# Performance work log

Hardware: AMD Instinct MI355X
Metric: run time of the kernel (lower is better)

## Reference

```python
import jax, jax.numpy as jnp
import numpy as np

K = 7        # kernal_size
STRIDE = 1
PAD = 3      # padding (reflect)
M = K // 2   # center tap index
GAMA = 0.5
EPS = 1e-09


def interp_linear(x, n_out):
    # torch F.interpolate(mode='linear', align_corners=False) on last dim. x: (b, c, n_in)
    n_in = x.shape[-1]
    src = (jnp.arange(n_out, dtype=jnp.float32) + 0.5) * (n_in / n_out) - 0.5
    src = jnp.clip(src, 0.0, n_in - 1.0)
    lo = jnp.floor(src).astype(jnp.int32)
    hi = jnp.minimum(lo + 1, n_in - 1)
    w = (src - lo.astype(jnp.float32)).astype(x.dtype)
    return x[..., lo] * (1.0 - w) + x[..., hi] * w


def unfold1d(x, k, s, p):
    # x: (b, c, n) -> windows (b, L, c, k), matching F.unfold's c-major/k-minor layout
    if p > 0:
        x = jnp.pad(x, ((0, 0), (0, 0), (p, p)), mode='reflect')
    n = x.shape[-1]
    L = (n - k) // s + 1
    idx = jnp.arange(L)[:, None] * s + jnp.arange(k)[None, :]  # (L, k)
    win = x[:, :, idx]                                          # (b, c, L, k)
    return jnp.transpose(win, (0, 2, 1, 3))                     # (b, L, c, k)


def setup_inputs() -> dict:
    key = jax.random.key(0)
    k1, k2, k3, k4, k5 = jax.random.split(key, 5)
    b, dc, nd = 16, 16, 1024
    c_in, c_out, n = 64, 128, 4096
    deep = jax.random.normal(k1, (b, dc, nd), dtype=jnp.float32)
    x = jax.random.normal(k2, (b, c_in, n), dtype=jnp.float32)
    conv_w = jax.random.normal(k3, (c_in, dc), dtype=jnp.float32) * (1.0 / np.sqrt(dc))
    conv_b = jax.random.normal(k4, (c_in,), dtype=jnp.float32) * 0.02
    fc_w = jax.random.normal(k5, (c_out, c_in * K), dtype=jnp.float32) * (1.0 / np.sqrt(c_in * K))
    return {"deep": deep, "x": x, "conv_w": conv_w, "conv_b": conv_b, "fc_w": fc_w}


def reference(deep, x, conv_w, conv_b, fc_w):
    b, c, n = x.shape
    # --- get_deep_loss ---
    xr = interp_linear(deep, n)                                  # (b, dc, n)
    y = jnp.einsum('bdn,cd->bcn', xr, conv_w) + conv_b[None, :, None]
    mean = jnp.mean(y, axis=2, keepdims=True)
    var = jnp.var(y, axis=2, keepdims=True, ddof=1)              # torch var_mean unbiased
    xs = GAMA * (y - mean) / (var + EPS)                         # DeepShuffle1d
    x1 = unfold1d(xs, K, STRIDE, PAD)                            # (b, L, c, k)
    d = jnp.abs(x1 - x1[..., M:M + 1])
    loss = 1.0 - jnp.tanh(d) ** 2                                # (b, L, c, k)
    alpha = 1.0 / jnp.sum(loss, axis=-1, keepdims=True)          # (b, L, c, 1)
    deep_loss = (loss * alpha).reshape(b, -1, c * K)             # (b, L, c*k)
    # --- deep_conv ---
    y1 = unfold1d(x, K, STRIDE, PAD).reshape(b, -1, c * K)       # (b, L, c*k)
    out = jnp.einsum('blf,of->bol', deep_loss * y1, fc_w)        # (b, c_out, L)
    return out
```

## Files before the change

kernel.cpp:

```cpp
#include <hip/hip_runtime.h>
#include <hip/hip_bf16.h>
#include <math.h>

namespace {
typedef __attribute__((ext_vector_type(8)))  short  short8;
typedef __attribute__((ext_vector_type(4)))  float  floatx4;

constexpr int Bc = 16;
constexpr int DC = 16;
constexpr int ND = 1024;
constexpr int C  = 64;
constexpr int N  = 4096;
constexpr int CO = 128;
constexpr int KW = 7;
constexpr int F  = C * KW;
constexpr int F2 = C * 8;
constexpr int LT = 32;
constexpr int PLD = F2 + 8;
constexpr int GPS = 560;
constexpr int NS = F2 / 32;

constexpr size_t WB_OFF = 0;
constexpr size_t GP_OFF = 262144;
constexpr size_t MC_OFF = 548864;
constexpr size_t SC_OFF = 552960;

constexpr float EXP2_SCALE = 2.8853900817779268f;

__device__ inline unsigned short f2bf(float f) {
    __hip_bfloat16 h = __float2bfloat16(f);
    return __builtin_bit_cast(unsigned short, h);
}
__device__ inline float rcpf(float x) { return __builtin_amdgcn_rcpf(x); }

__global__ __launch_bounds__(256)
void k0(const float* __restrict__ deep, const float* __restrict__ fcw,
        unsigned short* __restrict__ wbs, float* __restrict__ gp)
{
    __shared__ __align__(16) float Dch[DC][132];
    const int blk = blockIdx.x;
    const int tid = threadIdx.x;

    if (blk < 32) {
        const int g    = blk * 256 + tid;
        const int lane = g & 63;
        const int q    = lane >> 4;
        const int rr   = lane & 15;
        const int rest = g >> 6;
        const int t    = rest & 1;
        const int sw   = rest >> 1;
        const int s    = sw & 15;
        const int w    = sw >> 4;
        const int o    = w * 32 + t * 16 + rr;
        const int c    = s * 4 + q;
        const float* src = fcw + o * F + c * KW;
        const float4 v0 = *(const float4*)(src);
        const float4 v1 = *(const float4*)(src + 3);
        short8 h;
        h[0] = (short)f2bf(v0.x); h[1] = (short)f2bf(v0.y);
        h[2] = (short)f2bf(v0.z); h[3] = (short)f2bf(v0.w);
        h[4] = (short)f2bf(v1.y); h[5] = (short)f2bf(v1.z);
        h[6] = (short)f2bf(v1.w); h[7] = 0;
        ((short8*)wbs)[g] = h;
        return;
    }
    const int i2 = blk - 32;
    const int b  = i2 >> 3;
    const int ch = i2 & 7;
    const int t0 = ch * 128;
    const int d  = tid >> 4;
    const int e  = tid & 15;
#pragma unroll
    for (int p = 0; p < 9; ++p) {
        const int tt = e + 16 * p;
        if (tt < 129)
            Dch[d][tt] = deep[(b * DC + d) * ND + min(t0 + tt, ND - 1)];
    }
    __syncthreads();
    float a0 = 0.f, a1 = 0.f, as = 0.f;
    const int n1 = (ch == 7) ? 127 : 128;
    for (int t = 0; t < 128; ++t) {
        const float vd  = Dch[d][t];
        const float ve  = Dch[e][t];
        const float ve1 = (t < n1) ? Dch[e][t + 1] : 0.f;
        a0 = fmaf(vd, ve, a0);
        a1 = fmaf(vd, ve1, a1);
        as += vd;
    }
    float* gpb = gp + (b * 8 + ch) * GPS;
    gpb[tid] = a0;
    gpb[256 + tid] = a1;
    if (e == 0) {
        gpb[512 + d] = as;
        if (ch == 0) gpb[528 + d] = Dch[d][0];
        if (ch == 7) gpb[544 + d] = Dch[d][127];
    }
}

__global__ __launch_bounds__(256)
void ks(const float* __restrict__ gp, const float* __restrict__ conv_w,
        const float* __restrict__ conv_b, float* __restrict__ mcs,
        float* __restrict__ scs)
{
    __shared__ float G0s[256], G1s[256], ss[16], dd0[16], ddN[16], qp[8][64];
    const int b = blockIdx.x, tid = threadIdx.x;
    {
        float a0 = 0.f, a1 = 0.f;
#pragma unroll
        for (int ch = 0; ch < 8; ++ch) {
            const float* gpb = gp + (b * 8 + ch) * GPS;
            a0 += gpb[tid];
            a1 += gpb[256 + tid];
        }
        G0s[tid] = a0; G1s[tid] = a1;
        if (tid < 16) {
            float s = 0.f;
#pragma unroll
            for (int ch = 0; ch < 8; ++ch) s += gp[(b * 8 + ch) * GPS + 512 + tid];
            ss[tid]  = s;
            dd0[tid] = gp[(b * 8 + 0) * GPS + 528 + tid];
            ddN[tid] = gp[(b * 8 + 7) * GPS + 544 + tid];
        }
    }
    __syncthreads();
    const int c = tid & 63, part = tid >> 6;
    float w[DC];
    {
        const float4* wr = (const float4*)(conv_w + c * DC);
#pragma unroll
        for (int p = 0; p < 4; ++p) {
            const float4 v = wr[p];
            w[4 * p] = v.x; w[4 * p + 1] = v.y; w[4 * p + 2] = v.z; w[4 * p + 3] = v.w;
        }
    }
    float q0 = 0.f, q1 = 0.f;
#pragma unroll
    for (int dd = 0; dd < 4; ++dd) {
        const int d = 4 * part + dd;
        float i0 = 0.f, i1 = 0.f;
#pragma unroll
        for (int e = 0; e < DC; ++e) {
            i0 = fmaf(w[e], G0s[d * 16 + e], i0);
            i1 = fmaf(w[e], G1s[d * 16 + e], i1);
        }
        q0 = fmaf(w[d], i0, q0);
        q1 = fmaf(w[d], i1, q1);
    }
    qp[part][c] = q0;
    qp[4 + part][c] = q1;
    __syncthreads();
    if (tid < 64) {
        const float Q0 = qp[0][c] + qp[1][c] + qp[2][c] + qp[3][c];
        const float Q1 = qp[4][c] + qp[5][c] + qp[6][c] + qp[7][c];
        float wS = 0.f, V0 = 0.f, VN = 0.f;
#pragma unroll
        for (int d = 0; d < DC; ++d) {
            wS = fmaf(w[d], ss[d],  wS);
            V0 = fmaf(w[d], dd0[d], V0);
            VN = fmaf(w[d], ddN[d], VN);
        }
        const float cb   = conv_b[c];
        const float mean = wS * (1.f / 1024.f) + cb;
        const float S2   = 2.625f * Q0 + 1.375f * Q1 + 0.6875f * (V0 * V0 + VN * VN)
                         + 8.f * cb * wS + 4096.f * cb * cb;
        const float var  = (S2 - 4096.f * mean * mean) * (1.f / 4095.f);
        mcs[b * 64 + c] = wS * (1.f / 1024.f);
        scs[b * 64 + c] = (0.5f / (var + 1e-9f)) * EXP2_SCALE;
    }
}

__global__ __launch_bounds__(256, 3)
void k2(const float* __restrict__ deep, const float* __restrict__ conv_w,
        const float* __restrict__ x, const float* __restrict__ mcs,
        const float* __restrict__ scs, const unsigned short* __restrict__ wbs,
        float* __restrict__ out)
{
    __shared__ __align__(16) unsigned short phi[LT * PLD];
    __shared__ __align__(16) float Dw[12 * 16];
    const int b   = blockIdx.y;
    const int l0  = blockIdx.x * LT;
    const int t0  = l0 >> 2;
    const int tid = threadIdx.x;
    const int c   = tid & 63;
    const int seg = tid >> 6;

    if (tid < 192) {
        const int ti = tid >> 4, d = tid & 15;
        const int t = min(max(t0 - 2 + ti, 0), ND - 1);
        Dw[ti * 16 + d] = deep[(b * DC + d) * ND + t];
    }
    float w[DC];
    {
        const float4* wr = (const float4*)(conv_w + c * DC);
#pragma unroll
        for (int p = 0; p < 4; ++p) {
            const float4 v = wr[p];
            w[4 * p] = v.x; w[4 * p + 1] = v.y; w[4 * p + 2] = v.z; w[4 * p + 3] = v.w;
        }
    }
    const float mc  = mcs[b * 64 + c];
    const float sc2 = scs[b * 64 + c];

    const int base = l0 + seg * 8;
    const bool edge = (blockIdx.x == 0 && seg == 0) ||
                      (blockIdx.x == (N / LT - 1) && seg == 3);
    const float* xr = x + (size_t)(b * C + c) * N;
    float xf[16];
    if (!edge) {
        const float4 x0 = *(const float4*)(xr + base - 4);
        const float4 x1 = *(const float4*)(xr + base);
        const float4 x2 = *(const float4*)(xr + base + 4);
        const float4 x3 = *(const float4*)(xr + base + 8);
        xf[0]=x0.x; xf[1]=x0.y; xf[2]=x0.z; xf[3]=x0.w;
        xf[4]=x1.x; xf[5]=x1.y; xf[6]=x1.z; xf[7]=x1.w;
        xf[8]=x2.x; xf[9]=x2.y; xf[10]=x2.z; xf[11]=x2.w;
        xf[12]=x3.x; xf[13]=x3.y; xf[14]=x3.z; xf[15]=x3.w;
    }
    __syncthreads();

    {
        float Vr[6];
#pragma unroll
        for (int m = 0; m < 6; ++m) {
            const float* dr = Dw + (2 * seg + m) * 16;
            float a = 0.f;
#pragma unroll
            for (int d = 0; d < DC; ++d) a = fmaf(w[d], dr[d], a);
            Vr[m] = a;
        }
        const float WA[4] = {0.375f, 0.125f, 0.875f, 0.625f};
        float xsv[14], xvf[14];
        if (!edge) {
#pragma unroll
            for (int i = 0; i < 14; ++i) {
                const int r  = (i + 1) & 3;
                const int ma = ((i + 5) >> 2) - 1 + (r >> 1);
                const float wa = WA[r];
                xsv[i] = (fmaf(wa, Vr[ma], (1.f - wa) * Vr[ma + 1]) - mc) * sc2;
                xvf[i] = xf[1 + i];
            }
        } else {
            const int tbase = t0 + 2 * seg - 2;
#pragma unroll
            for (int i = 0; i < 14; ++i) {
                const int j  = base - 3 + i;
                const int ja = (j < 0) ? -j : j;
                const int jr = min(ja, 2 * N - 2 - ja);
                const int t  = jr >> 2;
                const int r  = jr & 3;
                const float wa = WA[r];
                int tA = t - 1 + (r >> 1);
                int tB = tA + 1;
                if (tA < 0) { tA = 0; tB = 0; }
                if (tB > ND - 1) tB = ND - 1;
                const int ia = tA - tbase;
                const int ib = tB - tbase;
                xsv[i] = (wa * Vr[ia] + (1.f - wa) * Vr[ib] - mc) * sc2;
                xvf[i] = xr[jr];
            }
        }
        unsigned short* pcol = phi + c * 8;
#pragma unroll
        for (int li = 0; li < 8; ++li) {
            const float cen = xsv[li + 3];
            float u[KW];
            float s = 0.25f;
            u[3] = 0.25f;
#pragma unroll
            for (int k = 0; k < KW; ++k) {
                if (k == 3) continue;
                const float d = fabsf(xsv[li + k] - cen);
                const float e = __builtin_amdgcn_exp2f(-d);
                const float t = 1.f + e;
                const float uk = e * rcpf(t * t);
                u[k] = uk;
                s += uk;
            }
            const float al = rcpf(s);
            short8 ph;
#pragma unroll
            for (int k = 0; k < KW; ++k) ph[k] = (short)f2bf(u[k] * al * xvf[li + k]);
            ph[7] = 0;
            *(short8*)(pcol + (seg * 8 + li) * PLD) = ph;
        }
    }
    __syncthreads();

    const int lane = tid & 63;
    const int quad = lane >> 4;
    const int rr   = lane & 15;
    const int o0   = seg * 32;

    floatx4 acc00 = {0.f, 0.f, 0.f, 0.f}, acc01 = acc00, acc10 = acc00, acc11 = acc00;
    const short8* wp = (const short8*)wbs + (size_t)seg * (NS * 2 * 64) + lane;
    const unsigned short* prow0 = phi + rr * PLD + quad * 8;
    const unsigned short* prow1 = prow0 + 16 * PLD;

#pragma unroll
    for (int s = 0; s < NS; ++s) {
        const int f0 = 32 * s;
        const short8 a0 = wp[s * 128];
        const short8 a1 = wp[s * 128 + 64];
        const short8 b0 = *(const short8*)(prow0 + f0);
        const short8 b1 = *(const short8*)(prow1 + f0);
        acc00 = __builtin_amdgcn_mfma_f32_16x16x32_bf16(a0, b0, acc00, 0, 0, 0);
        acc01 = __builtin_amdgcn_mfma_f32_16x16x32_bf16(a0, b1, acc01, 0, 0, 0);
        acc10 = __builtin_amdgcn_mfma_f32_16x16x32_bf16(a1, b0, acc10, 0, 0, 0);
        acc11 = __builtin_amdgcn_mfma_f32_16x16x32_bf16(a1, b1, acc11, 0, 0, 0);
    }

    float* ob = out + (size_t)(b * CO) * N + l0;
#pragma unroll
    for (int i = 0; i < 4; ++i) {
        const int om = quad * 4 + i;
        ob[(o0 + om) * N      + rr     ] = acc00[i];
        ob[(o0 + om) * N      + 16 + rr] = acc01[i];
        ob[(o0 + 16 + om) * N + rr     ] = acc10[i];
        ob[(o0 + 16 + om) * N + 16 + rr] = acc11[i];
    }
}
}

extern "C" void kernel_launch(void* const* d_in, const int* in_sizes, int n_in,
                              void* d_out, int out_size, void* d_ws, size_t ws_size,
                              hipStream_t stream)
{
    const float* deep   = (const float*)d_in[0];
    const float* x      = (const float*)d_in[1];
    const float* conv_w = (const float*)d_in[2];
    const float* conv_b = (const float*)d_in[3];
    const float* fc_w   = (const float*)d_in[4];
    float* out = (float*)d_out;

    unsigned short* wbuf = (unsigned short*)((char*)d_ws + WB_OFF);
    float*          gp   = (float*)((char*)d_ws + GP_OFF);
    float*          mcs  = (float*)((char*)d_ws + MC_OFF);
    float*          scs  = (float*)((char*)d_ws + SC_OFF);

    hipLaunchKernelGGL(k0, dim3(32 + 128), dim3(256), 0, stream,
                       deep, fc_w, wbuf, gp);
    hipLaunchKernelGGL(ks, dim3(Bc), dim3(256), 0, stream,
                       gp, conv_w, conv_b, mcs, scs);
    hipLaunchKernelGGL(k2, dim3(N / LT, Bc), dim3(256), 0, stream,
                       deep, conv_w, x, mcs, scs, wbuf, out);
}
```

Before: 115.8 us.

## Fold statistics kernel into main kernel and vectorize Gram and weight loops

Removes the separate per-batch statistics kernel. Every main-kernel block now reduces the partial Gram sums itself and derives the per-channel mean and scale in shared memory, which drops one launch and its serial dependency. Each of the 2048 blocks repeats this small reduction and adds two extra barriers and extra shared memory, which may lower occupancy. The Gram loop in k0 is also vectorized with float4 reads, and the tanh-derivative weights pair their reciprocals so one rcp serves two taps.

```diff
diff --git a/kernel.cpp b/kernel.cpp
--- a/kernel.cpp
+++ b/kernel.cpp
@@ -22,8 +22,6 @@
 
 constexpr size_t WB_OFF = 0;
 constexpr size_t GP_OFF = 262144;
-constexpr size_t MC_OFF = 548864;
-constexpr size_t SC_OFF = 552960;
 
 constexpr float EXP2_SCALE = 2.8853900817779268f;
 
@@ -77,15 +75,18 @@
             Dch[d][tt] = deep[(b * DC + d) * ND + min(t0 + tt, ND - 1)];
     }
     __syncthreads();
+    const bool inc3 = (ch != 7);
     float a0 = 0.f, a1 = 0.f, as = 0.f;
-    const int n1 = (ch == 7) ? 127 : 128;
-    for (int t = 0; t < 128; ++t) {
-        const float vd  = Dch[d][t];
-        const float ve  = Dch[e][t];
-        const float ve1 = (t < n1) ? Dch[e][t + 1] : 0.f;
-        a0 = fmaf(vd, ve, a0);
-        a1 = fmaf(vd, ve1, a1);
-        as += vd;
+    float4 Bn = *(const float4*)&Dch[e][0];
+#pragma unroll
+    for (int t = 0; t < 128; t += 4) {
+        const float4 A = *(const float4*)&Dch[d][t];
+        const float4 B = Bn;
+        Bn = *(const float4*)&Dch[e][t + 4];
+        a0 = fmaf(A.x, B.x, fmaf(A.y, B.y, fmaf(A.z, B.z, fmaf(A.w, B.w, a0))));
+        as += (A.x + A.y) + (A.z + A.w);
+        a1 = fmaf(A.x, B.y, fmaf(A.y, B.z, fmaf(A.z, B.w, a1)));
+        if (t < 124 || inc3) a1 = fmaf(A.w, Bn.x, a1);
     }
     float* gpb = gp + (b * 8 + ch) * GPS;
     gpb[tid] = a0;
@@ -97,86 +98,20 @@
     }
 }
 
-__global__ __launch_bounds__(256)
-void ks(const float* __restrict__ gp, const float* __restrict__ conv_w,
-        const float* __restrict__ conv_b, float* __restrict__ mcs,
-        float* __restrict__ scs)
-{
-    __shared__ float G0s[256], G1s[256], ss[16], dd0[16], ddN[16], qp[8][64];
-    const int b = blockIdx.x, tid = threadIdx.x;
-    {
-        float a0 = 0.f, a1 = 0.f;
-#pragma unroll
-        for (int ch = 0; ch < 8; ++ch) {
-            const float* gpb = gp + (b * 8 + ch) * GPS;
-            a0 += gpb[tid];
-            a1 += gpb[256 + tid];
-        }
-        G0s[tid] = a0; G1s[tid] = a1;
-        if (tid < 16) {
-            float s = 0.f;
-#pragma unroll
-            for (int ch = 0; ch < 8; ++ch) s += gp[(b * 8 + ch) * GPS + 512 + tid];
-            ss[tid]  = s;
-            dd0[tid] = gp[(b * 8 + 0) * GPS + 528 + tid];
-            ddN[tid] = gp[(b * 8 + 7) * GPS + 544 + tid];
-        }
-    }
-    __syncthreads();
-    const int c = tid & 63, part = tid >> 6;
-    float w[DC];
-    {
-        const float4* wr = (const float4*)(conv_w + c * DC);
-#pragma unroll
-        for (int p = 0; p < 4; ++p) {
-            const float4 v = wr[p];
-            w[4 * p] = v.x; w[4 * p + 1] = v.y; w[4 * p + 2] = v.z; w[4 * p + 3] = v.w;
-        }
-    }
-    float q0 = 0.f, q1 = 0.f;
-#pragma unroll
-    for (int dd = 0; dd < 4; ++dd) {
-        const int d = 4 * part + dd;
-        float i0 = 0.f, i1 = 0.f;
-#pragma unroll
-        for (int e = 0; e < DC; ++e) {
-            i0 = fmaf(w[e], G0s[d * 16 + e], i0);
-            i1 = fmaf(w[e], G1s[d * 16 + e], i1);
-        }
-        q0 = fmaf(w[d], i0, q0);
-        q1 = fmaf(w[d], i1, q1);
-    }
-    qp[part][c] = q0;
-    qp[4 + part][c] = q1;
-    __syncthreads();
-    if (tid < 64) {
-        const float Q0 = qp[0][c] + qp[1][c] + qp[2][c] + qp[3][c];
-        const float Q1 = qp[4][c] + qp[5][c] + qp[6][c] + qp[7][c];
-        float wS = 0.f, V0 = 0.f, VN = 0.f;
-#pragma unroll
-        for (int d = 0; d < DC; ++d) {
-            wS = fmaf(w[d], ss[d],  wS);
-            V0 = fmaf(w[d], dd0[d], V0);
-            VN = fmaf(w[d], ddN[d], VN);
-        }
-        const float cb   = conv_b[c];
-        const float mean = wS * (1.f / 1024.f) + cb;
-        const float S2   = 2.625f * Q0 + 1.375f * Q1 + 0.6875f * (V0 * V0 + VN * VN)
-                         + 8.f * cb * wS + 4096.f * cb * cb;
-        const float var  = (S2 - 4096.f * mean * mean) * (1.f / 4095.f);
-        mcs[b * 64 + c] = wS * (1.f / 1024.f);
-        scs[b * 64 + c] = (0.5f / (var + 1e-9f)) * EXP2_SCALE;
-    }
-}
-
 __global__ __launch_bounds__(256, 3)
 void k2(const float* __restrict__ deep, const float* __restrict__ conv_w,
-        const float* __restrict__ x, const float* __restrict__ mcs,
-        const float* __restrict__ scs, const unsigned short* __restrict__ wbs,
+        const float* __restrict__ conv_b, const float* __restrict__ x,
+        const float* __restrict__ gp, const unsigned short* __restrict__ wbs,
         float* __restrict__ out)
 {
     __shared__ __align__(16) unsigned short phi[LT * PLD];
     __shared__ __align__(16) float Dw[12 * 16];
+    __shared__ __align__(16) float G0s[256];
+    __shared__ __align__(16) float G1s[256];
+    __shared__ float ssL[16], dd0L[16], ddNL[16];
+    __shared__ float qp[8][64];
+    __shared__ float mcL[64], scL[64];
+
     const int b   = blockIdx.y;
     const int l0  = blockIdx.x * LT;
     const int t0  = l0 >> 2;
@@ -184,10 +119,26 @@
     const int c   = tid & 63;
     const int seg = tid >> 6;
 
+    const float* gpB = gp + (size_t)(b * 8) * GPS;
+    float a0 = 0.f, a1 = 0.f;
+#pragma unroll
+    for (int ch = 0; ch < 8; ++ch) {
+        a0 += gpB[ch * GPS + tid];
+        a1 += gpB[ch * GPS + 256 + tid];
+    }
+    float sA = 0.f, d0v = 0.f, dNv = 0.f;
+    if (tid < 16) {
+#pragma unroll
+        for (int ch = 0; ch < 8; ++ch) sA += gpB[ch * GPS + 512 + tid];
+        d0v = gpB[528 + tid];
+        dNv = gpB[7 * GPS + 544 + tid];
+    }
+    const float cb = (tid < 64) ? conv_b[c] : 0.f;
+
     if (tid < 192) {
-        const int ti = tid >> 4, d = tid & 15;
+        const int ti = tid >> 4, dd = tid & 15;
         const int t = min(max(t0 - 2 + ti, 0), ND - 1);
-        Dw[ti * 16 + d] = deep[(b * DC + d) * ND + t];
+        Dw[ti * 16 + dd] = deep[(b * DC + dd) * ND + t];
     }
     float w[DC];
     {
@@ -198,8 +149,6 @@
             w[4 * p] = v.x; w[4 * p + 1] = v.y; w[4 * p + 2] = v.z; w[4 * p + 3] = v.w;
         }
     }
-    const float mc  = mcs[b * 64 + c];
-    const float sc2 = scs[b * 64 + c];
 
     const int base = l0 + seg * 8;
     const bool edge = (blockIdx.x == 0 && seg == 0) ||
@@ -216,16 +165,68 @@
         xf[8]=x2.x; xf[9]=x2.y; xf[10]=x2.z; xf[11]=x2.w;
         xf[12]=x3.x; xf[13]=x3.y; xf[14]=x3.z; xf[15]=x3.w;
     }
-    __syncthreads();
+
+    G0s[tid] = a0; G1s[tid] = a1;
+    if (tid < 16) { ssL[tid] = sA; dd0L[tid] = d0v; ddNL[tid] = dNv; }
+    __syncthreads();
+
+    {
+        float q0 = 0.f, q1 = 0.f;
+#pragma unroll
+        for (int dd = 0; dd < 4; ++dd) {
+            const int d = 4 * seg + dd;
+            const float4* g0r = (const float4*)(G0s + d * 16);
+            const float4* g1r = (const float4*)(G1s + d * 16);
+            float i0 = 0.f, i1 = 0.f;
+#pragma unroll
+            for (int p = 0; p < 4; ++p) {
+                const float4 v0 = g0r[p];
+                const float4 v1 = g1r[p];
+                i0 = fmaf(w[4*p],   v0.x, i0); i0 = fmaf(w[4*p+1], v0.y, i0);
+                i0 = fmaf(w[4*p+2], v0.z, i0); i0 = fmaf(w[4*p+3], v0.w, i0);
+                i1 = fmaf(w[4*p],   v1.x, i1); i1 = fmaf(w[4*p+1], v1.y, i1);
+                i1 = fmaf(w[4*p+2], v1.z, i1); i1 = fmaf(w[4*p+3], v1.w, i1);
+            }
+            q0 = fmaf(w[d], i0, q0);
+            q1 = fmaf(w[d], i1, q1);
+        }
+        qp[seg][c] = q0;
+        qp[4 + seg][c] = q1;
+    }
+    __syncthreads();
+    if (tid < 64) {
+        const float Q0 = qp[0][c] + qp[1][c] + qp[2][c] + qp[3][c];
+        const float Q1 = qp[4][c] + qp[5][c] + qp[6][c] + qp[7][c];
+        float wS = 0.f, V0 = 0.f, VN = 0.f;
+#pragma unroll
+        for (int d = 0; d < DC; ++d) {
+            wS = fmaf(w[d], ssL[d],  wS);
+            V0 = fmaf(w[d], dd0L[d], V0);
+            VN = fmaf(w[d], ddNL[d], VN);
+        }
+        const float mean = wS * (1.f / 1024.f) + cb;
+        const float S2   = 2.625f * Q0 + 1.375f * Q1 + 0.6875f * (V0 * V0 + VN * VN)
+                         + 8.f * cb * wS + 4096.f * cb * cb;
+        const float var  = (S2 - 4096.f * mean * mean) * (1.f / 4095.f);
+        mcL[c] = wS * (1.f / 1024.f);
+        scL[c] = (0.5f / (var + 1e-9f)) * EXP2_SCALE;
+    }
+    __syncthreads();
+    const float mc  = mcL[c];
+    const float sc2 = scL[c];
 
     {
         float Vr[6];
 #pragma unroll
         for (int m = 0; m < 6; ++m) {
-            const float* dr = Dw + (2 * seg + m) * 16;
+            const float4* dr4 = (const float4*)(Dw + (2 * seg + m) * 16);
             float a = 0.f;
 #pragma unroll
-            for (int d = 0; d < DC; ++d) a = fmaf(w[d], dr[d], a);
+            for (int p = 0; p < 4; ++p) {
+                const float4 v = dr4[p];
+                a = fmaf(w[4*p],   v.x, a); a = fmaf(w[4*p+1], v.y, a);
+                a = fmaf(w[4*p+2], v.z, a); a = fmaf(w[4*p+3], v.w, a);
+            }
             Vr[m] = a;
         }
         const float WA[4] = {0.375f, 0.125f, 0.875f, 0.625f};
@@ -263,18 +264,28 @@
 #pragma unroll
         for (int li = 0; li < 8; ++li) {
             const float cen = xsv[li + 3];
-            float u[KW];
-            float s = 0.25f;
-            u[3] = 0.25f;
-#pragma unroll
-            for (int k = 0; k < KW; ++k) {
-                if (k == 3) continue;
+            float ev[6], t2[6];
+#pragma unroll
+            for (int j = 0; j < 6; ++j) {
+                const int k = (j < 3) ? j : j + 1;
                 const float d = fabsf(xsv[li + k] - cen);
                 const float e = __builtin_amdgcn_exp2f(-d);
                 const float t = 1.f + e;
-                const float uk = e * rcpf(t * t);
-                u[k] = uk;
-                s += uk;
+                ev[j] = e; t2[j] = t * t;
+            }
+            float u[KW];
+            u[3] = 0.25f;
+            float s = 0.25f;
+#pragma unroll
+            for (int pr = 0; pr < 3; ++pr) {
+                const int ja = 2 * pr, jb = 2 * pr + 1;
+                const float r  = rcpf(t2[ja] * t2[jb]);
+                const float ua = ev[ja] * t2[jb] * r;
+                const float ub = ev[jb] * t2[ja] * r;
+                const int ka = (ja < 3) ? ja : ja + 1;
+                const int kb = (jb < 3) ? jb : jb + 1;
+                u[ka] = ua; u[kb] = ub;
+                s += ua + ub;
             }
             const float al = rcpf(s);
             short8 ph;
@@ -299,14 +310,14 @@
 #pragma unroll
     for (int s = 0; s < NS; ++s) {
         const int f0 = 32 * s;
-        const short8 a0 = wp[s * 128];
-        const short8 a1 = wp[s * 128 + 64];
-        const short8 b0 = *(const short8*)(prow0 + f0);
-        const short8 b1 = *(const short8*)(prow1 + f0);
-        acc00 = __builtin_amdgcn_mfma_f32_16x16x32_bf16(a0, b0, acc00, 0, 0, 0);
-        acc01 = __builtin_amdgcn_mfma_f32_16x16x32_bf16(a0, b1, acc01, 0, 0, 0);
-        acc10 = __builtin_amdgcn_mfma_f32_16x16x32_bf16(a1, b0, acc10, 0, 0, 0);
-        acc11 = __builtin_amdgcn_mfma_f32_16x16x32_bf16(a1, b1, acc11, 0, 0, 0);
+        const short8 a0f = wp[s * 128];
+        const short8 a1f = wp[s * 128 + 64];
+        const short8 b0f = *(const short8*)(prow0 + f0);
+        const short8 b1f = *(const short8*)(prow1 + f0);
+        acc00 = __builtin_amdgcn_mfma_f32_16x16x32_bf16(a0f, b0f, acc00, 0, 0, 0);
+        acc01 = __builtin_amdgcn_mfma_f32_16x16x32_bf16(a0f, b1f, acc01, 0, 0, 0);
+        acc10 = __builtin_amdgcn_mfma_f32_16x16x32_bf16(a1f, b0f, acc10, 0, 0, 0);
+        acc11 = __builtin_amdgcn_mfma_f32_16x16x32_bf16(a1f, b1f, acc11, 0, 0, 0);
     }
 
     float* ob = out + (size_t)(b * CO) * N + l0;
@@ -334,13 +345,9 @@
 
     unsigned short* wbuf = (unsigned short*)((char*)d_ws + WB_OFF);
     float*          gp   = (float*)((char*)d_ws + GP_OFF);
-    float*          mcs  = (float*)((char*)d_ws + MC_OFF);
-    float*          scs  = (float*)((char*)d_ws + SC_OFF);
 
     hipLaunchKernelGGL(k0, dim3(32 + 128), dim3(256), 0, stream,
                        deep, fc_w, wbuf, gp);
-    hipLaunchKernelGGL(ks, dim3(Bc), dim3(256), 0, stream,
-                       gp, conv_w, conv_b, mcs, scs);
     hipLaunchKernelGGL(k2, dim3(N / LT, Bc), dim3(256), 0, stream,
-                       deep, conv_w, x, mcs, scs, wbuf, out);
-}
+                       deep, conv_w, conv_b, x, gp, wbuf, out);
+}
```

Measured after the change: 109.8 us. 5.2% less time.
